# Kernel tuning notes

Measured on AMD Instinct MI355X. Metric: run time of the kernel, lower is better.

Reference implementation:

```python
import jax, jax.numpy as jnp
import numpy as np

HEAD_NUM = 16
EMBED_DIM = 1024
HIDDEN_DIM = 1024
HEAD_DIM = HIDDEN_DIM // HEAD_NUM


def setup_inputs() -> dict:
    key = jax.random.key(0)
    ks = jax.random.split(key, 7)
    B, S = 2, 2048
    X = jax.random.normal(ks[0], (B, S, EMBED_DIM), dtype=jnp.float32)
    sc = 1.0 / np.sqrt(EMBED_DIM)
    Wq = jax.random.normal(ks[1], (EMBED_DIM, HIDDEN_DIM), dtype=jnp.float32) * sc
    Wk = jax.random.normal(ks[2], (EMBED_DIM, HIDDEN_DIM), dtype=jnp.float32) * sc
    Wv = jax.random.normal(ks[3], (EMBED_DIM, HIDDEN_DIM), dtype=jnp.float32) * sc
    bq = jax.random.normal(ks[4], (HIDDEN_DIM,), dtype=jnp.float32) * 0.01
    bk = jax.random.normal(ks[5], (HIDDEN_DIM,), dtype=jnp.float32) * 0.01
    bv = jax.random.normal(ks[6], (HIDDEN_DIM,), dtype=jnp.float32) * 0.01
    return {"X": X, "Wq": Wq, "bq": bq, "Wk": Wk, "bk": bk, "Wv": Wv, "bv": bv}


def reference(X, Wq, bq, Wk, bk, Wv, bv):
    B, S, _ = X.shape
    # projections -> [B, H, S, D]
    def split_heads(t):
        return t.reshape(B, S, HEAD_NUM, HEAD_DIM).transpose(0, 2, 1, 3)
    Q = split_heads(X @ Wq + bq)
    K = split_heads(X @ Wk + bk)  # computed but unused, faithful to source bug
    V = split_heads(X @ Wv + bv)
    # NOTE: source computes Q @ V^T (bug), reproduced faithfully
    scores = jnp.einsum('bhqd,bhkd->bhqk', Q, V) / np.sqrt(HEAD_DIM)
    attn = jax.nn.softmax(scores, axis=-1)  # dropout is identity in eval
    out = jnp.einsum('bhqk,bhkd->bhqd', attn, V)
    return out.transpose(0, 2, 1, 3).reshape(B, S, HIDDEN_DIM)
```

## Files before the change

kernel.cpp:

```cpp
#include <hip/hip_runtime.h>
#include <math.h>


constexpr int BATCH = 2;
constexpr int SEQ   = 2048;
constexpr int EMB   = 1024;
constexpr int NHEAD = 16;
constexpr int HDIM  = 64;
constexpr int HID   = 1024;

typedef __attribute__((ext_vector_type(8))) _Float16 half8;
typedef __attribute__((ext_vector_type(4))) float    f32x4;

#define MFMA16(a, b, c) __builtin_amdgcn_mfma_f32_16x16x32_f16((a), (b), (c), 0, 0, 0)

constexpr int LDT = 72;

__device__ __forceinline__ int vt_idx(int d, int k) {
    return (d << 6) + ((((k >> 3) + (d >> 3)) & 7) << 3) + (k & 7);
}

__device__ __forceinline__ _Float16 f2h(float f) { return (_Float16)f; }

__global__ __launch_bounds__(256) void conv_x_kernel(
    const float* __restrict__ X, _Float16* __restrict__ Xb, int n4)
{
    union Pack { uint2 q; _Float16 e[4]; };
    int idx = blockIdx.x * 256 + threadIdx.x;
    int stride = gridDim.x * 256;
    for (int i = idx; i < n4; i += stride) {
        float4 v = ((const float4*)X)[i];
        Pack p;
        p.e[0] = f2h(v.x); p.e[1] = f2h(v.y);
        p.e[2] = f2h(v.z); p.e[3] = f2h(v.w);
        ((uint2*)Xb)[i] = p.q;
    }
}

__global__ __launch_bounds__(256) void conv_wt_kernel(
    const float* __restrict__ W, _Float16* __restrict__ WT)
{
    __shared__ _Float16 T[64 * 68];
    const int tid = threadIdx.x;
    const int n0 = blockIdx.x * 64;
    const int k0 = blockIdx.y * 64;

    #pragma unroll
    for (int i = 0; i < 4; ++i) {
        const int u = tid + i * 256;
        const int r = u >> 4;
        const int c4 = (u & 15) << 2;
        const float4 v = *(const float4*)&W[(size_t)(k0 + r) * HID + n0 + c4];
        T[r * 68 + c4 + 0] = f2h(v.x);
        T[r * 68 + c4 + 1] = f2h(v.y);
        T[r * 68 + c4 + 2] = f2h(v.z);
        T[r * 68 + c4 + 3] = f2h(v.w);
    }
    __syncthreads();

    union Pack { uint4 q; _Float16 e[8]; };
    #pragma unroll
    for (int i = 0; i < 2; ++i) {
        const int u = tid + i * 256;
        const int n = u >> 3;
        const int kc = (u & 7) << 3;
        Pack p;
        #pragma unroll
        for (int j = 0; j < 8; ++j) p.e[j] = T[(kc + j) * 68 + n];
        *(uint4*)&WT[(size_t)(n0 + n) * EMB + k0 + kc] = p.q;
    }
}

__global__ __launch_bounds__(256) void proj_kernel(
    const _Float16* __restrict__ Xb, const _Float16* __restrict__ WTq,
    const _Float16* __restrict__ WTv, const float* __restrict__ bq,
    const float* __restrict__ bv, _Float16* __restrict__ Qo,
    _Float16* __restrict__ Vo)
{
    __shared__ __align__(16) _Float16 Xs[128 * LDT];
    __shared__ __align__(16) _Float16 Wqs[64 * LDT];
    __shared__ __align__(16) _Float16 Wvs[64 * LDT];

    const int tid  = threadIdx.x;
    const int lane = tid & 63;
    const int w    = tid >> 6;
    const int h    = blockIdx.x;
    const int m0   = blockIdx.y * 128;
    const int n0   = h * HDIM;
    const int l15  = lane & 15;
    const int l4   = lane >> 4;

    f32x4 aq[2][4], av[2][4];
    #pragma unroll
    for (int mt = 0; mt < 2; ++mt)
        #pragma unroll
        for (int nt = 0; nt < 4; ++nt) {
            aq[mt][nt] = f32x4{0.f, 0.f, 0.f, 0.f};
            av[mt][nt] = f32x4{0.f, 0.f, 0.f, 0.f};
        }

    for (int k0 = 0; k0 < EMB; k0 += 64) {
        #pragma unroll
        for (int i = 0; i < 4; ++i) {
            const int u = tid + i * 256;
            const int r = u >> 3;
            const int c8 = (u & 7) << 3;
            *(uint4*)&Xs[r * LDT + c8] =
                *(const uint4*)&Xb[(size_t)(m0 + r) * EMB + k0 + c8];
        }
        #pragma unroll
        for (int i = 0; i < 2; ++i) {
            const int u = tid + i * 256;
            const int r = u >> 3;
            const int c8 = (u & 7) << 3;
            *(uint4*)&Wqs[r * LDT + c8] =
                *(const uint4*)&WTq[(size_t)(n0 + r) * EMB + k0 + c8];
            *(uint4*)&Wvs[r * LDT + c8] =
                *(const uint4*)&WTv[(size_t)(n0 + r) * EMB + k0 + c8];
        }
        __syncthreads();

        #pragma unroll
        for (int kd = 0; kd < 2; ++kd) {
            const int ko = kd * 32 + l4 * 8;
            half8 xa0 = *(const half8*)&Xs[(w * 32 + l15) * LDT + ko];
            half8 xa1 = *(const half8*)&Xs[(w * 32 + 16 + l15) * LDT + ko];
            #pragma unroll
            for (int nt = 0; nt < 4; ++nt) {
                half8 wq = *(const half8*)&Wqs[(nt * 16 + l15) * LDT + ko];
                half8 wv = *(const half8*)&Wvs[(nt * 16 + l15) * LDT + ko];
                aq[0][nt] = MFMA16(xa0, wq, aq[0][nt]);
                aq[1][nt] = MFMA16(xa1, wq, aq[1][nt]);
                av[0][nt] = MFMA16(xa0, wv, av[0][nt]);
                av[1][nt] = MFMA16(xa1, wv, av[1][nt]);
            }
        }
        __syncthreads();
    }

    #pragma unroll
    for (int nt = 0; nt < 4; ++nt) {
        const float bqv = bq[n0 + nt * 16 + l15];
        const float bvv = bv[n0 + nt * 16 + l15];
        #pragma unroll
        for (int mt = 0; mt < 2; ++mt)
            #pragma unroll
            for (int r = 0; r < 4; ++r) {
                const int m = m0 + w * 32 + mt * 16 + l4 * 4 + r;
                const int bb = m >> 11;
                const int s  = m & (SEQ - 1);
                const size_t base =
                    ((size_t)(bb * NHEAD + h) * SEQ + s) * HDIM + nt * 16 + l15;
                Qo[base] = f2h(aq[mt][nt][r] + bqv);
                Vo[base] = f2h(av[mt][nt][r] + bvv);
            }
    }
}

__global__ __launch_bounds__(256) void attn_kernel(
    const _Float16* __restrict__ Qw, const _Float16* __restrict__ Vw,
    float* __restrict__ out)
{
    __shared__ __align__(16) _Float16 Qs[64 * LDT];
    __shared__ __align__(16) _Float16 Vs[64 * LDT];
    __shared__ __align__(16) _Float16 VTs[64 * 64];
    __shared__ __align__(16) _Float16 Ps[64 * LDT];

    const int tid  = threadIdx.x;
    const int lane = tid & 63;
    const int w    = tid >> 6;
    const int l15  = lane & 15;
    const int l4   = lane >> 4;
    const int qb   = blockIdx.x;
    const int bh   = blockIdx.y;
    const int b    = bh >> 4;
    const int h    = bh & (NHEAD - 1);
    const int s0   = qb * 64;

    const _Float16* Qp = Qw + (size_t)bh * SEQ * HDIM;
    const _Float16* Vp = Vw + (size_t)bh * SEQ * HDIM;

    union Pack { uint4 q; _Float16 e[8]; };

    auto stageV = [&](int t) {
        #pragma unroll
        for (int i = 0; i < 2; ++i) {
            const int u = tid + i * 256;
            const int r = u >> 3;
            const int c8 = (u & 7) << 3;
            Pack p;
            p.q = *(const uint4*)&Vp[(size_t)(t * 64 + r) * HDIM + c8];
            *(uint4*)&Vs[r * LDT + c8] = p.q;
            #pragma unroll
            for (int j = 0; j < 8; ++j)
                VTs[vt_idx(c8 + j, r)] = p.e[j];
        }
    };

    #pragma unroll
    for (int i = 0; i < 2; ++i) {
        const int u = tid + i * 256;
        const int r = u >> 3;
        const int c8 = (u & 7) << 3;
        *(uint4*)&Qs[r * LDT + c8] =
            *(const uint4*)&Qp[(size_t)(s0 + r) * HDIM + c8];
    }
    stageV(0);
    __syncthreads();

    const half8 qa0 = *(const half8*)&Qs[(w * 16 + l15) * LDT + l4 * 8];
    const half8 qa1 = *(const half8*)&Qs[(w * 16 + l15) * LDT + 32 + l4 * 8];

    f32x4 acc_o[4];
    #pragma unroll
    for (int dt = 0; dt < 4; ++dt) acc_o[dt] = f32x4{0.f, 0.f, 0.f, 0.f};
    float m_i[4] = {-INFINITY, -INFINITY, -INFINITY, -INFINITY};
    float l_i[4] = {0.f, 0.f, 0.f, 0.f};

    const int prow_base = (w * 16 + l4 * 4) * LDT + l15;
    const int pa_row = (w * 16 + l15) * LDT;

    for (int t = 0; t < SEQ / 64; ++t) {
        f32x4 acc_s[4];
        #pragma unroll
        for (int nt = 0; nt < 4; ++nt) acc_s[nt] = f32x4{0.f, 0.f, 0.f, 0.f};
        #pragma unroll
        for (int nt = 0; nt < 4; ++nt) {
            half8 vb0 = *(const half8*)&Vs[(nt * 16 + l15) * LDT + l4 * 8];
            half8 vb1 = *(const half8*)&Vs[(nt * 16 + l15) * LDT + 32 + l4 * 8];
            acc_s[nt] = MFMA16(qa0, vb0, acc_s[nt]);
            acc_s[nt] = MFMA16(qa1, vb1, acc_s[nt]);
        }

        #pragma unroll
        for (int r = 0; r < 4; ++r) {
            float sA = acc_s[0][r] * 0.125f;
            float sB = acc_s[1][r] * 0.125f;
            float sC = acc_s[2][r] * 0.125f;
            float sD = acc_s[3][r] * 0.125f;
            float mloc = fmaxf(fmaxf(sA, sB), fmaxf(sC, sD));
            #pragma unroll
            for (int off = 1; off < 16; off <<= 1)
                mloc = fmaxf(mloc, __shfl_xor(mloc, off));
            const float mnew = fmaxf(m_i[r], mloc);
            const float corr = __expf(m_i[r] - mnew);
            const float p0 = __expf(sA - mnew);
            const float p1 = __expf(sB - mnew);
            const float p2 = __expf(sC - mnew);
            const float p3 = __expf(sD - mnew);
            float rs = (p0 + p1) + (p2 + p3);
            #pragma unroll
            for (int off = 1; off < 16; off <<= 1)
                rs += __shfl_xor(rs, off);
            l_i[r] = l_i[r] * corr + rs;
            m_i[r] = mnew;
            const int pr = prow_base + r * LDT;
            Ps[pr +  0] = f2h(p0);
            Ps[pr + 16] = f2h(p1);
            Ps[pr + 32] = f2h(p2);
            Ps[pr + 48] = f2h(p3);
            acc_o[0][r] *= corr; acc_o[1][r] *= corr;
            acc_o[2][r] *= corr; acc_o[3][r] *= corr;
        }

        half8 pa0 = *(const half8*)&Ps[pa_row + l4 * 8];
        half8 pa1 = *(const half8*)&Ps[pa_row + 32 + l4 * 8];
        #pragma unroll
        for (int dt = 0; dt < 4; ++dt) {
            const int d = dt * 16 + l15;
            half8 vt0 = *(const half8*)&VTs[vt_idx(d, l4 * 8)];
            half8 vt1 = *(const half8*)&VTs[vt_idx(d, 32 + l4 * 8)];
            acc_o[dt] = MFMA16(pa0, vt0, acc_o[dt]);
            acc_o[dt] = MFMA16(pa1, vt1, acc_o[dt]);
        }

        __syncthreads();
        if (t + 1 < SEQ / 64) {
            stageV(t + 1);
            __syncthreads();
        }
    }

    #pragma unroll
    for (int r = 0; r < 4; ++r) {
        const float inv = 1.f / l_i[r];
        const int s = s0 + w * 16 + l4 * 4 + r;
        float* op = &out[((size_t)(b * SEQ + s)) * HID + h * HDIM + l15];
        op[ 0] = acc_o[0][r] * inv;
        op[16] = acc_o[1][r] * inv;
        op[32] = acc_o[2][r] * inv;
        op[48] = acc_o[3][r] * inv;
    }
}

extern "C" void kernel_launch(void* const* d_in, const int* in_sizes, int n_in,
                              void* d_out, int out_size, void* d_ws, size_t ws_size,
                              hipStream_t stream) {
    (void)in_sizes; (void)n_in; (void)out_size; (void)ws_size;
    const float* X  = (const float*)d_in[0];
    const float* Wq = (const float*)d_in[1];
    const float* bq = (const float*)d_in[2];
    const float* Wv = (const float*)d_in[5];
    const float* bv = (const float*)d_in[6];
    float* outp = (float*)d_out;

    char* ws = (char*)d_ws;
    _Float16* Xb  = (_Float16*)(ws);
    _Float16* WTq = (_Float16*)(ws + 8388608);
    _Float16* WTv = (_Float16*)(ws + 8388608 + 2097152);
    _Float16* Qb  = (_Float16*)(ws + 12582912);
    _Float16* Vb  = (_Float16*)(ws + 20971520);

    conv_x_kernel<<<2048, 256, 0, stream>>>(X, Xb, (BATCH * SEQ * EMB) / 4);
    conv_wt_kernel<<<dim3(16, 16), 256, 0, stream>>>(Wq, WTq);
    conv_wt_kernel<<<dim3(16, 16), 256, 0, stream>>>(Wv, WTv);
    proj_kernel<<<dim3(NHEAD, (BATCH * SEQ) / 128), 256, 0, stream>>>(
        Xb, WTq, WTv, bq, bv, Qb, Vb);
    attn_kernel<<<dim3(SEQ / 64, BATCH * NHEAD), 256, 0, stream>>>(Qb, Vb, outp);
}
```

Baseline: 247.4 us.

## Emit transposed V from projection, swizzle P buffer, remap workgroups, add setprio

The projection kernel now also writes a transposed copy of V to global memory, so the attention kernel can stage V^T with vector loads instead of scalar shared-memory scatters. The attention kernel reuses the Q shared buffer for P with an XOR swizzle, widens the LDS row pitch, and wraps the MFMA blocks in s_setprio. Both kernels use a 1D grid with a remapped block index, likely to spread related blocks across XCDs for L2 locality. The cost is extra global writes of V^T in the projection, which uses strided scalar stores.

```diff
diff --git a/kernel.cpp b/kernel.cpp
--- a/kernel.cpp
+++ b/kernel.cpp
@@ -14,11 +14,7 @@
 
 #define MFMA16(a, b, c) __builtin_amdgcn_mfma_f32_16x16x32_f16((a), (b), (c), 0, 0, 0)
 
-constexpr int LDT = 72;
-
-__device__ __forceinline__ int vt_idx(int d, int k) {
-    return (d << 6) + ((((k >> 3) + (d >> 3)) & 7) << 3) + (k & 7);
-}
+constexpr int LDT = 80;
 
 __device__ __forceinline__ _Float16 f2h(float f) { return (_Float16)f; }
 
@@ -75,7 +71,7 @@
     const _Float16* __restrict__ Xb, const _Float16* __restrict__ WTq,
     const _Float16* __restrict__ WTv, const float* __restrict__ bq,
     const float* __restrict__ bv, _Float16* __restrict__ Qo,
-    _Float16* __restrict__ Vo)
+    _Float16* __restrict__ Vo, _Float16* __restrict__ VTo)
 {
     __shared__ __align__(16) _Float16 Xs[128 * LDT];
     __shared__ __align__(16) _Float16 Wqs[64 * LDT];
@@ -84,8 +80,10 @@
     const int tid  = threadIdx.x;
     const int lane = tid & 63;
     const int w    = tid >> 6;
-    const int h    = blockIdx.x;
-    const int m0   = blockIdx.y * 128;
+    const int wg   = blockIdx.x;
+    const int nid  = (wg & 7) * 64 + (wg >> 3);
+    const int h    = nid >> 5;
+    const int m0   = (nid & 31) * 128;
     const int n0   = h * HDIM;
     const int l15  = lane & 15;
     const int l4   = lane >> 4;
@@ -120,6 +118,7 @@
         }
         __syncthreads();
 
+        __builtin_amdgcn_s_setprio(1);
         #pragma unroll
         for (int kd = 0; kd < 2; ++kd) {
             const int ko = kd * 32 + l4 * 8;
@@ -135,13 +134,15 @@
                 av[1][nt] = MFMA16(xa1, wv, av[1][nt]);
             }
         }
+        __builtin_amdgcn_s_setprio(0);
         __syncthreads();
     }
 
     #pragma unroll
     for (int nt = 0; nt < 4; ++nt) {
-        const float bqv = bq[n0 + nt * 16 + l15];
-        const float bvv = bv[n0 + nt * 16 + l15];
+        const int d = nt * 16 + l15;
+        const float bqv = bq[n0 + d];
+        const float bvv = bv[n0 + d];
         #pragma unroll
         for (int mt = 0; mt < 2; ++mt)
             #pragma unroll
@@ -149,38 +150,39 @@
                 const int m = m0 + w * 32 + mt * 16 + l4 * 4 + r;
                 const int bb = m >> 11;
                 const int s  = m & (SEQ - 1);
-                const size_t base =
-                    ((size_t)(bb * NHEAD + h) * SEQ + s) * HDIM + nt * 16 + l15;
-                Qo[base] = f2h(aq[mt][nt][r] + bqv);
-                Vo[base] = f2h(av[mt][nt][r] + bvv);
+                const int bh = bb * NHEAD + h;
+                const float vval = av[mt][nt][r] + bvv;
+                Qo[((size_t)bh * SEQ + s) * HDIM + d] = f2h(aq[mt][nt][r] + bqv);
+                Vo[((size_t)bh * SEQ + s) * HDIM + d] = f2h(vval);
+                VTo[((size_t)bh * HDIM + d) * SEQ + s] = f2h(vval);
             }
     }
 }
 
 __global__ __launch_bounds__(256) void attn_kernel(
     const _Float16* __restrict__ Qw, const _Float16* __restrict__ Vw,
-    float* __restrict__ out)
+    const _Float16* __restrict__ VTw, float* __restrict__ out)
 {
-    __shared__ __align__(16) _Float16 Qs[64 * LDT];
+    __shared__ __align__(16) _Float16 PQs[64 * LDT];
     __shared__ __align__(16) _Float16 Vs[64 * LDT];
-    __shared__ __align__(16) _Float16 VTs[64 * 64];
-    __shared__ __align__(16) _Float16 Ps[64 * LDT];
+    __shared__ __align__(16) _Float16 VTs[64 * LDT];
 
     const int tid  = threadIdx.x;
     const int lane = tid & 63;
     const int w    = tid >> 6;
     const int l15  = lane & 15;
     const int l4   = lane >> 4;
-    const int qb   = blockIdx.x;
-    const int bh   = blockIdx.y;
-    const int b    = bh >> 4;
-    const int h    = bh & (NHEAD - 1);
-    const int s0   = qb * 64;
-
-    const _Float16* Qp = Qw + (size_t)bh * SEQ * HDIM;
-    const _Float16* Vp = Vw + (size_t)bh * SEQ * HDIM;
-
-    union Pack { uint4 q; _Float16 e[8]; };
+    const int wg = blockIdx.x;
+    const int nw = (wg & 7) * 128 + (wg >> 3);
+    const int bh = nw >> 5;
+    const int qb = nw & 31;
+    const int b  = bh >> 4;
+    const int h  = bh & (NHEAD - 1);
+    const int s0 = qb * 64;
+
+    const _Float16* Qp  = Qw  + (size_t)bh * SEQ * HDIM;
+    const _Float16* Vp  = Vw  + (size_t)bh * SEQ * HDIM;
+    const _Float16* VTp = VTw + (size_t)bh * HDIM * SEQ;
 
     auto stageV = [&](int t) {
         #pragma unroll
@@ -188,12 +190,10 @@
             const int u = tid + i * 256;
             const int r = u >> 3;
             const int c8 = (u & 7) << 3;
-            Pack p;
-            p.q = *(const uint4*)&Vp[(size_t)(t * 64 + r) * HDIM + c8];
-            *(uint4*)&Vs[r * LDT + c8] = p.q;
-            #pragma unroll
-            for (int j = 0; j < 8; ++j)
-                VTs[vt_idx(c8 + j, r)] = p.e[j];
+            *(uint4*)&Vs[r * LDT + c8] =
+                *(const uint4*)&Vp[(size_t)(t * 64 + r) * HDIM + c8];
+            *(uint4*)&VTs[r * LDT + c8] =
+                *(const uint4*)&VTp[(size_t)r * SEQ + t * 64 + c8];
         }
     };
 
@@ -202,14 +202,14 @@
         const int u = tid + i * 256;
         const int r = u >> 3;
         const int c8 = (u & 7) << 3;
-        *(uint4*)&Qs[r * LDT + c8] =
+        *(uint4*)&PQs[r * LDT + c8] =
             *(const uint4*)&Qp[(size_t)(s0 + r) * HDIM + c8];
     }
     stageV(0);
     __syncthreads();
 
-    const half8 qa0 = *(const half8*)&Qs[(w * 16 + l15) * LDT + l4 * 8];
-    const half8 qa1 = *(const half8*)&Qs[(w * 16 + l15) * LDT + 32 + l4 * 8];
+    const half8 qa0 = *(const half8*)&PQs[(w * 16 + l15) * LDT + l4 * 8];
+    const half8 qa1 = *(const half8*)&PQs[(w * 16 + l15) * LDT + 32 + l4 * 8];
 
     f32x4 acc_o[4];
     #pragma unroll
@@ -217,13 +217,15 @@
     float m_i[4] = {-INFINITY, -INFINITY, -INFINITY, -INFINITY};
     float l_i[4] = {0.f, 0.f, 0.f, 0.f};
 
-    const int prow_base = (w * 16 + l4 * 4) * LDT + l15;
-    const int pa_row = (w * 16 + l15) * LDT;
+    const int chi  = l15 >> 3;
+    const int hl   = l15 & 7;
+    const int rkey = l15 & 7;
 
     for (int t = 0; t < SEQ / 64; ++t) {
         f32x4 acc_s[4];
         #pragma unroll
         for (int nt = 0; nt < 4; ++nt) acc_s[nt] = f32x4{0.f, 0.f, 0.f, 0.f};
+        __builtin_amdgcn_s_setprio(1);
         #pragma unroll
         for (int nt = 0; nt < 4; ++nt) {
             half8 vb0 = *(const half8*)&Vs[(nt * 16 + l15) * LDT + l4 * 8];
@@ -231,6 +233,7 @@
             acc_s[nt] = MFMA16(qa0, vb0, acc_s[nt]);
             acc_s[nt] = MFMA16(qa1, vb1, acc_s[nt]);
         }
+        __builtin_amdgcn_s_setprio(0);
 
         #pragma unroll
         for (int r = 0; r < 4; ++r) {
@@ -254,25 +257,28 @@
                 rs += __shfl_xor(rs, off);
             l_i[r] = l_i[r] * corr + rs;
             m_i[r] = mnew;
-            const int pr = prow_base + r * LDT;
-            Ps[pr +  0] = f2h(p0);
-            Ps[pr + 16] = f2h(p1);
-            Ps[pr + 32] = f2h(p2);
-            Ps[pr + 48] = f2h(p3);
+            const int key = (l4 * 4 + r) & 7;
+            _Float16* pr = &PQs[(w * 16 + l4 * 4 + r) * LDT];
+            pr[(((0 + chi) ^ key) << 3) + hl] = f2h(p0);
+            pr[(((2 + chi) ^ key) << 3) + hl] = f2h(p1);
+            pr[(((4 + chi) ^ key) << 3) + hl] = f2h(p2);
+            pr[(((6 + chi) ^ key) << 3) + hl] = f2h(p3);
             acc_o[0][r] *= corr; acc_o[1][r] *= corr;
             acc_o[2][r] *= corr; acc_o[3][r] *= corr;
         }
 
-        half8 pa0 = *(const half8*)&Ps[pa_row + l4 * 8];
-        half8 pa1 = *(const half8*)&Ps[pa_row + 32 + l4 * 8];
+        const _Float16* prd = &PQs[(w * 16 + l15) * LDT];
+        half8 pa0 = *(const half8*)&prd[((l4 ^ rkey) << 3)];
+        half8 pa1 = *(const half8*)&prd[(((4 + l4) ^ rkey) << 3)];
+        __builtin_amdgcn_s_setprio(1);
         #pragma unroll
         for (int dt = 0; dt < 4; ++dt) {
-            const int d = dt * 16 + l15;
-            half8 vt0 = *(const half8*)&VTs[vt_idx(d, l4 * 8)];
-            half8 vt1 = *(const half8*)&VTs[vt_idx(d, 32 + l4 * 8)];
+            half8 vt0 = *(const half8*)&VTs[(dt * 16 + l15) * LDT + l4 * 8];
+            half8 vt1 = *(const half8*)&VTs[(dt * 16 + l15) * LDT + 32 + l4 * 8];
             acc_o[dt] = MFMA16(pa0, vt0, acc_o[dt]);
             acc_o[dt] = MFMA16(pa1, vt1, acc_o[dt]);
         }
+        __builtin_amdgcn_s_setprio(0);
 
         __syncthreads();
         if (t + 1 < SEQ / 64) {
@@ -306,15 +312,15 @@
 
     char* ws = (char*)d_ws;
     _Float16* Xb  = (_Float16*)(ws);
-    _Float16* WTq = (_Float16*)(ws + 8388608);
-    _Float16* WTv = (_Float16*)(ws + 8388608 + 2097152);
-    _Float16* Qb  = (_Float16*)(ws + 12582912);
-    _Float16* Vb  = (_Float16*)(ws + 20971520);
+    _Float16* WTq = (_Float16*)(ws + (8u  << 20));
+    _Float16* WTv = (_Float16*)(ws + (10u << 20));
+    _Float16* Qb  = (_Float16*)(ws + (12u << 20));
+    _Float16* Vb  = (_Float16*)(ws + (20u << 20));
+    _Float16* VTb = (_Float16*)(ws + (28u << 20));
 
     conv_x_kernel<<<2048, 256, 0, stream>>>(X, Xb, (BATCH * SEQ * EMB) / 4);
     conv_wt_kernel<<<dim3(16, 16), 256, 0, stream>>>(Wq, WTq);
     conv_wt_kernel<<<dim3(16, 16), 256, 0, stream>>>(Wv, WTv);
-    proj_kernel<<<dim3(NHEAD, (BATCH * SEQ) / 128), 256, 0, stream>>>(
-        Xb, WTq, WTv, bq, bv, Qb, Vb);
-    attn_kernel<<<dim3(SEQ / 64, BATCH * NHEAD), 256, 0, stream>>>(Qb, Vb, outp);
-}
+    proj_kernel<<<512, 256, 0, stream>>>(Xb, WTq, WTv, bq, bv, Qb, Vb, VTb);
+    attn_kernel<<<1024, 256, 0, stream>>>(Qb, Vb, VTb, outp);
+}
```

New measurement: 218.5 us. 11.7% less time.
